# Kernel optimization log

Measured on AMD Instinct MI355X. Metric: run time of the kernel, lower is better.

Reference implementation:

```python
import jax, jax.numpy as jnp
import numpy as np

T = 200000


def _sine_layer(tvec, A, w, phi, phic, wc):
    # tvec: (t,), A/w/phi: (n,1), phic/wc: (1,)
    phi_static = jax.nn.relu(phic)  # (1,)
    w_static = jax.nn.relu(wc)
    ph = jax.nn.relu(phi) + phi_static  # (n,1)
    ww = jax.nn.relu(w) + w_static
    sine = A * jnp.sin(ww * tvec[None, :] + ph)  # (n,t)
    return sine, phi_static, w_static


def _selector_layer(tvec, wave_input, w, phi, phic, wc, phi_prev, w_prev):
    # wave_input: (n,t), w/phi: (m,n), phic/wc/phi_prev/w_prev: (1,)
    # NOTE: phi_prev/w_prev passed but phi_prev flag is False in the network,
    # so they are NOT added (matches torch: `if self.phi_prev and ...`).
    phi_static = jax.nn.relu(phic)
    w_static = jax.nn.relu(wc)
    ph = (jax.nn.relu(phi) + phi_static)[:, :, None]  # (m,n,1)
    ww = (jax.nn.relu(w) + w_static)[:, :, None]
    sine = 0.5 * jnp.sin(ww * tvec[None, None, :] + ph) + 0.5  # (m,n,t)
    out = jnp.einsum('mnt,nt->mt', sine, wave_input)  # (m,t)
    return out, phi_static, w_static


def setup_inputs() -> dict:
    key = jax.random.key(0)
    ks = jax.random.split(key, 18)
    r = lambda k, s: jax.random.normal(k, s, dtype=jnp.float32)
    return {
        'initial_wave_input': r(ks[0], (20, T)),
        'A0': r(ks[1], (20, 1)), 'w0': r(ks[2], (20, 1)), 'phi0': r(ks[3], (20, 1)),
        'wc0': r(ks[4], (1,)), 'phic0': r(ks[5], (1,)),
        'w1': r(ks[6], (25, 20)), 'phi1': r(ks[7], (25, 20)),
        'wc1': r(ks[8], (1,)), 'phic1': r(ks[9], (1,)),
        'w2': r(ks[10], (30, 25)), 'phi2': r(ks[11], (30, 25)),
        'wc2': r(ks[12], (1,)), 'phic2': r(ks[13], (1,)),
        'w3': r(ks[14], (1, 30)), 'phi3': r(ks[15], (1, 30)),
        'wc3': r(ks[16], (1,)), 'phic3': r(ks[17], (1,)),
    }


def reference(initial_wave_input, A0, w0, phi0, wc0, phic0,
              w1, phi1, wc1, phic1, w2, phi2, wc2, phic2,
              w3, phi3, wc3, phic3):
    tvec = jnp.linspace(1.0, 1000.0, T, dtype=jnp.float32)
    # initial_wave_input is an argument of the torch module but is never used.
    s, phi, w = _sine_layer(tvec, A0, w0, phi0, phic0, wc0)
    s, phi, w = _selector_layer(tvec, s, w1, phi1, phic1, wc1, phi, w)
    s, phi, w = _selector_layer(tvec, s, w2, phi2, phic2, wc2, phi, w)
    s, phi, w = _selector_layer(tvec, s, w3, phi3, phic3, wc3, phi, w)
    return s  # (1, t)
```

## Files before the change

kernel.cpp:

```cpp
#include <hip/hip_runtime.h>
#include <hip/hip_bf16.h>

#define T_TOTAL 200000
#define INV2PI 0.15915494309189535f

__device__ float g_P[2840];

__device__ __forceinline__ float relu_f(float x) { return fmaxf(x, 0.0f); }

__device__ __forceinline__ float sin_rev(float rev) {
    return __builtin_amdgcn_sinf(__builtin_amdgcn_fractf(rev));
}

__global__ void prep_kernel(
    const float* __restrict__ A0,
    const float* __restrict__ w0, const float* __restrict__ phi0,
    const float* __restrict__ wc0, const float* __restrict__ phic0,
    const float* __restrict__ w1, const float* __restrict__ phi1,
    const float* __restrict__ wc1, const float* __restrict__ phic1,
    const float* __restrict__ w2, const float* __restrict__ phi2,
    const float* __restrict__ wc2, const float* __restrict__ phic2,
    const float* __restrict__ w3, const float* __restrict__ phi3,
    const float* __restrict__ wc3, const float* __restrict__ phic3)
{
    const int tid = blockIdx.x * blockDim.x + threadIdx.x;
    const int stride = blockDim.x * gridDim.x;

    const float ws0 = relu_f(wc0[0]), ps0 = relu_f(phic0[0]);
    const float ws1 = relu_f(wc1[0]), ps1 = relu_f(phic1[0]);
    const float ws2 = relu_f(wc2[0]), ps2 = relu_f(phic2[0]);
    const float ws3 = relu_f(wc3[0]), ps3 = relu_f(phic3[0]);

    for (int n = tid; n < 20; n += stride) {
        g_P[2 * n]     = (relu_f(w0[n])   + ws0) * INV2PI;
        g_P[2 * n + 1] = (relu_f(phi0[n]) + ps0) * INV2PI;
        g_P[40 + n]    = A0[n];
    }
    for (int k = tid; k < 20 * 28; k += stride) {
        const int n = k / 28, m = k % 28;
        const int d = 60 + 2 * k;
        if (m < 25) {
            const int s = m * 20 + n;
            g_P[d]     = (relu_f(w1[s])   + ws1) * INV2PI;
            g_P[d + 1] = (relu_f(phi1[s]) + ps1) * INV2PI;
        } else {
            g_P[d] = 0.0f; g_P[d + 1] = 0.0f;
        }
    }
    for (int k = tid; k < 25 * 32; k += stride) {
        const int n = k / 32, m = k % 32;
        const int d = 1180 + 2 * k;
        if (m < 30) {
            const int s = m * 25 + n;
            g_P[d]     = (relu_f(w2[s])   + ws2) * INV2PI;
            g_P[d + 1] = (relu_f(phi2[s]) + ps2) * INV2PI;
        } else {
            g_P[d] = 0.0f; g_P[d + 1] = 0.0f;
        }
    }
    for (int k = tid; k < 30; k += stride) {
        g_P[2780 + 2 * k]     = (relu_f(w3[k])   + ws3) * INV2PI;
        g_P[2780 + 2 * k + 1] = (relu_f(phi3[k]) + ps3) * INV2PI;
    }
}

__launch_bounds__(256)
__global__ void wave_main(float* __restrict__ out)
{
    __shared__ float sh0[20 * 64];
    __shared__ float sh1[25 * 64];
    __shared__ float sh2[30 * 64];

    const int tid = threadIdx.x;
    const int l = tid & 63;
    const int w = __builtin_amdgcn_readfirstlane(tid >> 6);
    const int t = blockIdx.x * 64 + l;
    const float tv = fmaf((float)t, 999.0f / 199999.0f, 1.0f);

    {
        const float* __restrict__ p = &g_P[10 * w];
        const float* __restrict__ a = &g_P[40 + 5 * w];
#pragma unroll
        for (int i = 0; i < 5; ++i) {
            float rev = fmaf(p[2 * i], tv, p[2 * i + 1]);
            sh0[(5 * w + i) * 64 + l] = a[i] * sin_rev(rev);
        }
    }
    __syncthreads();

    float acc1[7];
#pragma unroll
    for (int j = 0; j < 7; ++j) acc1[j] = 0.0f;
    float sum0 = 0.0f;
#pragma clang loop unroll(disable)
    for (int n = 0; n < 20; ++n) {
        const float s0n = sh0[n * 64 + l];
        sum0 += s0n;
        const float* __restrict__ p = &g_P[60 + 56 * n + 14 * w];
#pragma unroll
        for (int j = 0; j < 7; ++j) {
            float rev = fmaf(p[2 * j], tv, p[2 * j + 1]);
            acc1[j] = fmaf(sin_rev(rev), s0n, acc1[j]);
        }
    }
#pragma unroll
    for (int j = 0; j < 7; ++j) {
        const int m = 7 * w + j;
        if (m < 25) sh1[m * 64 + l] = fmaf(0.5f, acc1[j], 0.5f * sum0);
    }
    __syncthreads();

    float acc2[8];
#pragma unroll
    for (int j = 0; j < 8; ++j) acc2[j] = 0.0f;
    float sum1 = 0.0f;
#pragma clang loop unroll(disable)
    for (int n = 0; n < 25; ++n) {
        const float s1n = sh1[n * 64 + l];
        sum1 += s1n;
        const float* __restrict__ p = &g_P[1180 + 64 * n + 16 * w];
#pragma unroll
        for (int j = 0; j < 8; ++j) {
            float rev = fmaf(p[2 * j], tv, p[2 * j + 1]);
            acc2[j] = fmaf(sin_rev(rev), s1n, acc2[j]);
        }
    }
#pragma unroll
    for (int j = 0; j < 8; ++j) {
        const int m = 8 * w + j;
        if (m < 30) sh2[m * 64 + l] = fmaf(0.5f, acc2[j], 0.5f * sum1);
    }
    __syncthreads();

    if (w == 0) {
        float acc3 = 0.0f, sum2 = 0.0f;
#pragma unroll
        for (int n = 0; n < 30; ++n) {
            const float s2n = sh2[n * 64 + l];
            sum2 += s2n;
            float rev = fmaf(g_P[2780 + 2 * n], tv, g_P[2780 + 2 * n + 1]);
            acc3 = fmaf(sin_rev(rev), s2n, acc3);
        }
        out[t] = fmaf(0.5f, acc3, 0.5f * sum2);
    }
}

extern "C" void kernel_launch(void* const* d_in, const int* in_sizes, int n_in,
                              void* d_out, int out_size, void* d_ws, size_t ws_size,
                              hipStream_t stream) {
    (void)in_sizes; (void)n_in; (void)d_ws; (void)ws_size; (void)out_size;
    const float* A0    = (const float*)d_in[1];
    const float* w0    = (const float*)d_in[2];
    const float* phi0  = (const float*)d_in[3];
    const float* wc0   = (const float*)d_in[4];
    const float* phic0 = (const float*)d_in[5];
    const float* w1    = (const float*)d_in[6];
    const float* phi1  = (const float*)d_in[7];
    const float* wc1   = (const float*)d_in[8];
    const float* phic1 = (const float*)d_in[9];
    const float* w2    = (const float*)d_in[10];
    const float* phi2  = (const float*)d_in[11];
    const float* wc2   = (const float*)d_in[12];
    const float* phic2 = (const float*)d_in[13];
    const float* w3    = (const float*)d_in[14];
    const float* phi3  = (const float*)d_in[15];
    const float* wc3   = (const float*)d_in[16];
    const float* phic3 = (const float*)d_in[17];

    float* out = (float*)d_out;

    hipLaunchKernelGGL(prep_kernel, dim3(11), dim3(256), 0, stream,
                       A0, w0, phi0, wc0, phic0,
                       w1, phi1, wc1, phic1,
                       w2, phi2, wc2, phic2,
                       w3, phi3, wc3, phic3);

    const int grid = T_TOTAL / 64;
    hipLaunchKernelGGL(wave_main, dim3(grid), dim3(256), 0, stream, out);
}
```

Before: 53.51 us.

## Use Chebyshev recurrence and polynomial sine with 4 time points per thread

Each thread now handles four time samples spaced 64 apart. It computes sin directly for the first two and gets the other two from the recurrence x_{k+1} = 2cos(wΔ)x_k − x_{k−1}, using cosines precomputed in double on the device. The hardware sin is replaced by a minimax polynomial on the fractional revolution, with a quarter-turn phase offset baked in. The last layer's dot product is split across all four waves and reduced through shared memory. This cuts transcendental work and grid size, at the cost of approximation error and error growth in the recurrence, especially at the large phase arguments used.

```diff
diff --git a/kernel.cpp b/kernel.cpp
--- a/kernel.cpp
+++ b/kernel.cpp
@@ -2,14 +2,20 @@
 #include <hip/hip_bf16.h>
 
 #define T_TOTAL 200000
-#define INV2PI 0.15915494309189535f
-
-__device__ float g_P[2840];
-
-__device__ __forceinline__ float relu_f(float x) { return fmaxf(x, 0.0f); }
-
-__device__ __forceinline__ float sin_rev(float rev) {
-    return __builtin_amdgcn_sinf(__builtin_amdgcn_fractf(rev));
+
+typedef float v4f __attribute__((ext_vector_type(4)));
+
+__device__ float g_P[4496];
+
+__device__ __forceinline__ float sinp(float rev) {
+    float g = __builtin_amdgcn_fractf(rev);
+    float h = g - 0.5f;
+    float u = h * h;
+    float p = fmaf(45.621248f, u, -82.391040f);
+    p = fmaf(p, u, 64.671616f);
+    p = fmaf(p, u, -19.730960f);
+    p = fmaf(p, u, 0.9999618f);
+    return p;
 }
 
 __global__ void prep_kernel(
@@ -26,123 +32,176 @@
     const int tid = blockIdx.x * blockDim.x + threadIdx.x;
     const int stride = blockDim.x * gridDim.x;
 
-    const float ws0 = relu_f(wc0[0]), ps0 = relu_f(phic0[0]);
-    const float ws1 = relu_f(wc1[0]), ps1 = relu_f(phic1[0]);
-    const float ws2 = relu_f(wc2[0]), ps2 = relu_f(phic2[0]);
-    const float ws3 = relu_f(wc3[0]), ps3 = relu_f(phic3[0]);
+    const double I2PI = 0.15915494309189535;
+    const double D64  = 64.0 * 999.0 / 199999.0;
+
+    const double ws0 = fmax((double)wc0[0], 0.0), ps0 = fmax((double)phic0[0], 0.0);
+    const double ws1 = fmax((double)wc1[0], 0.0), ps1 = fmax((double)phic1[0], 0.0);
+    const double ws2 = fmax((double)wc2[0], 0.0), ps2 = fmax((double)phic2[0], 0.0);
+    const double ws3 = fmax((double)wc3[0], 0.0), ps3 = fmax((double)phic3[0], 0.0);
 
     for (int n = tid; n < 20; n += stride) {
-        g_P[2 * n]     = (relu_f(w0[n])   + ws0) * INV2PI;
-        g_P[2 * n + 1] = (relu_f(phi0[n]) + ps0) * INV2PI;
-        g_P[40 + n]    = A0[n];
-    }
-    for (int k = tid; k < 20 * 28; k += stride) {
-        const int n = k / 28, m = k % 28;
-        const int d = 60 + 2 * k;
+        double wr = fmax((double)w0[n], 0.0) + ws0;
+        g_P[n]      = (float)(wr * I2PI);
+        g_P[20 + n] = (float)((fmax((double)phi0[n], 0.0) + ps0) * I2PI + 0.25);
+        g_P[40 + n] = (float)(2.0 * cos(wr * D64));
+        g_P[60 + n] = A0[n];
+    }
+    for (int k = tid; k < 20 * 32; k += stride) {
+        const int n = k >> 5, m = k & 31;
+        float wwf = 0.0f, phf = 0.25f, cf = 2.0f;
         if (m < 25) {
             const int s = m * 20 + n;
-            g_P[d]     = (relu_f(w1[s])   + ws1) * INV2PI;
-            g_P[d + 1] = (relu_f(phi1[s]) + ps1) * INV2PI;
-        } else {
-            g_P[d] = 0.0f; g_P[d + 1] = 0.0f;
-        }
+            double wr = fmax((double)w1[s], 0.0) + ws1;
+            wwf = (float)(wr * I2PI);
+            phf = (float)((fmax((double)phi1[s], 0.0) + ps1) * I2PI + 0.25);
+            cf  = (float)(2.0 * cos(wr * D64));
+        }
+        g_P[80 + 96 * n + m]      = wwf;
+        g_P[80 + 96 * n + 32 + m] = phf;
+        g_P[80 + 96 * n + 64 + m] = cf;
     }
     for (int k = tid; k < 25 * 32; k += stride) {
-        const int n = k / 32, m = k % 32;
-        const int d = 1180 + 2 * k;
+        const int n = k >> 5, m = k & 31;
+        float wwf = 0.0f, phf = 0.25f, cf = 2.0f;
         if (m < 30) {
             const int s = m * 25 + n;
-            g_P[d]     = (relu_f(w2[s])   + ws2) * INV2PI;
-            g_P[d + 1] = (relu_f(phi2[s]) + ps2) * INV2PI;
-        } else {
-            g_P[d] = 0.0f; g_P[d + 1] = 0.0f;
-        }
-    }
-    for (int k = tid; k < 30; k += stride) {
-        g_P[2780 + 2 * k]     = (relu_f(w3[k])   + ws3) * INV2PI;
-        g_P[2780 + 2 * k + 1] = (relu_f(phi3[k]) + ps3) * INV2PI;
+            double wr = fmax((double)w2[s], 0.0) + ws2;
+            wwf = (float)(wr * I2PI);
+            phf = (float)((fmax((double)phi2[s], 0.0) + ps2) * I2PI + 0.25);
+            cf  = (float)(2.0 * cos(wr * D64));
+        }
+        g_P[2000 + 96 * n + m]      = wwf;
+        g_P[2000 + 96 * n + 32 + m] = phf;
+        g_P[2000 + 96 * n + 64 + m] = cf;
+    }
+    for (int k = tid; k < 32; k += stride) {
+        float wwf = 0.0f, phf = 0.0f, cf = 2.0f;
+        if (k < 30) {
+            double wr = fmax((double)w3[k], 0.0) + ws3;
+            wwf = (float)(wr * I2PI);
+            phf = (float)((fmax((double)phi3[k], 0.0) + ps3) * I2PI + 0.25);
+            cf  = (float)(2.0 * cos(wr * D64));
+        }
+        g_P[4400 + k]      = wwf;
+        g_P[4400 + 32 + k] = phf;
+        g_P[4400 + 64 + k] = cf;
     }
 }
 
 __launch_bounds__(256)
 __global__ void wave_main(float* __restrict__ out)
 {
-    __shared__ float sh0[20 * 64];
-    __shared__ float sh1[25 * 64];
-    __shared__ float sh2[30 * 64];
-
-    const int tid = threadIdx.x;
-    const int l = tid & 63;
-    const int w = __builtin_amdgcn_readfirstlane(tid >> 6);
-    const int t = blockIdx.x * 64 + l;
-    const float tv = fmaf((float)t, 999.0f / 199999.0f, 1.0f);
-
-    {
-        const float* __restrict__ p = &g_P[10 * w];
-        const float* __restrict__ a = &g_P[40 + 5 * w];
-#pragma unroll
-        for (int i = 0; i < 5; ++i) {
-            float rev = fmaf(p[2 * i], tv, p[2 * i + 1]);
-            sh0[(5 * w + i) * 64 + l] = a[i] * sin_rev(rev);
-        }
+    __shared__ float sh0[20][64][4];
+    __shared__ float sh1[25][64][4];
+    __shared__ float shp[4][64][4];
+
+    const int l = threadIdx.x & 63;
+    const int w = __builtin_amdgcn_readfirstlane(threadIdx.x >> 6);
+    const int tb = blockIdx.x * 256;
+    const float STEP = 999.0f / 199999.0f;
+
+    float tv[4];
+#pragma unroll
+    for (int j = 0; j < 4; ++j)
+        tv[j] = fmaf((float)(tb + l + 64 * j), STEP, 1.0f);
+
+#pragma unroll
+    for (int i = 0; i < 5; ++i) {
+        const int n = 5 * w + i;
+        const float ww = g_P[n], ph = g_P[20 + n], C = g_P[40 + n], A = g_P[60 + n];
+        float x0 = A * sinp(fmaf(ww, tv[0], ph));
+        float x1 = A * sinp(fmaf(ww, tv[1], ph));
+        float x2 = fmaf(C, x1, -x0);
+        float x3 = fmaf(C, x2, -x1);
+        *(v4f*)&sh0[n][l][0] = (v4f){x0, x1, x2, x3};
     }
     __syncthreads();
 
-    float acc1[7];
-#pragma unroll
-    for (int j = 0; j < 7; ++j) acc1[j] = 0.0f;
-    float sum0 = 0.0f;
+    float acc1[8][4] = {};
+    float sum0[4] = {0.f, 0.f, 0.f, 0.f};
 #pragma clang loop unroll(disable)
     for (int n = 0; n < 20; ++n) {
-        const float s0n = sh0[n * 64 + l];
-        sum0 += s0n;
-        const float* __restrict__ p = &g_P[60 + 56 * n + 14 * w];
-#pragma unroll
-        for (int j = 0; j < 7; ++j) {
-            float rev = fmaf(p[2 * j], tv, p[2 * j + 1]);
-            acc1[j] = fmaf(sin_rev(rev), s0n, acc1[j]);
-        }
-    }
-#pragma unroll
-    for (int j = 0; j < 7; ++j) {
-        const int m = 7 * w + j;
-        if (m < 25) sh1[m * 64 + l] = fmaf(0.5f, acc1[j], 0.5f * sum0);
+        const v4f s0 = *(const v4f*)&sh0[n][l][0];
+#pragma unroll
+        for (int j = 0; j < 4; ++j) sum0[j] += s0[j];
+        const float* __restrict__ pb = &g_P[80 + 96 * n + 8 * w];
+#pragma unroll
+        for (int k = 0; k < 8; ++k) {
+            const float ww = pb[k], ph = pb[32 + k], C = pb[64 + k];
+            float x0 = sinp(fmaf(ww, tv[0], ph));
+            float x1 = sinp(fmaf(ww, tv[1], ph));
+            float x2 = fmaf(C, x1, -x0);
+            float x3 = fmaf(C, x2, -x1);
+            acc1[k][0] = fmaf(x0, s0[0], acc1[k][0]);
+            acc1[k][1] = fmaf(x1, s0[1], acc1[k][1]);
+            acc1[k][2] = fmaf(x2, s0[2], acc1[k][2]);
+            acc1[k][3] = fmaf(x3, s0[3], acc1[k][3]);
+        }
+    }
+#pragma unroll
+    for (int k = 0; k < 8; ++k) {
+        if (8 * w + k < 25) {
+            v4f v;
+#pragma unroll
+            for (int j = 0; j < 4; ++j) v[j] = fmaf(0.5f, acc1[k][j], 0.5f * sum0[j]);
+            *(v4f*)&sh1[8 * w + k][l][0] = v;
+        }
     }
     __syncthreads();
 
-    float acc2[8];
-#pragma unroll
-    for (int j = 0; j < 8; ++j) acc2[j] = 0.0f;
-    float sum1 = 0.0f;
+    float acc2[8][4] = {};
+    float sum1[4] = {0.f, 0.f, 0.f, 0.f};
 #pragma clang loop unroll(disable)
     for (int n = 0; n < 25; ++n) {
-        const float s1n = sh1[n * 64 + l];
-        sum1 += s1n;
-        const float* __restrict__ p = &g_P[1180 + 64 * n + 16 * w];
-#pragma unroll
-        for (int j = 0; j < 8; ++j) {
-            float rev = fmaf(p[2 * j], tv, p[2 * j + 1]);
-            acc2[j] = fmaf(sin_rev(rev), s1n, acc2[j]);
-        }
-    }
-#pragma unroll
-    for (int j = 0; j < 8; ++j) {
-        const int m = 8 * w + j;
-        if (m < 30) sh2[m * 64 + l] = fmaf(0.5f, acc2[j], 0.5f * sum1);
-    }
+        const v4f s1 = *(const v4f*)&sh1[n][l][0];
+#pragma unroll
+        for (int j = 0; j < 4; ++j) sum1[j] += s1[j];
+        const float* __restrict__ pb = &g_P[2000 + 96 * n + 8 * w];
+#pragma unroll
+        for (int k = 0; k < 8; ++k) {
+            const float ww = pb[k], ph = pb[32 + k], C = pb[64 + k];
+            float x0 = sinp(fmaf(ww, tv[0], ph));
+            float x1 = sinp(fmaf(ww, tv[1], ph));
+            float x2 = fmaf(C, x1, -x0);
+            float x3 = fmaf(C, x2, -x1);
+            acc2[k][0] = fmaf(x0, s1[0], acc2[k][0]);
+            acc2[k][1] = fmaf(x1, s1[1], acc2[k][1]);
+            acc2[k][2] = fmaf(x2, s1[2], acc2[k][2]);
+            acc2[k][3] = fmaf(x3, s1[3], acc2[k][3]);
+        }
+    }
+    float s2r[8][4];
+#pragma unroll
+    for (int k = 0; k < 8; ++k)
+#pragma unroll
+        for (int j = 0; j < 4; ++j)
+            s2r[k][j] = fmaf(0.5f, acc2[k][j], 0.5f * sum1[j]);
+
+    float pw[4] = {0.f, 0.f, 0.f, 0.f};
+    {
+        const float* __restrict__ pb = &g_P[4400 + 8 * w];
+#pragma unroll
+        for (int k = 0; k < 8; ++k) {
+            if (8 * w + k < 30) {
+                const float ww = pb[k], ph = pb[32 + k], C = pb[64 + k];
+                float x0 = sinp(fmaf(ww, tv[0], ph));
+                float x1 = sinp(fmaf(ww, tv[1], ph));
+                float x2 = fmaf(C, x1, -x0);
+                float x3 = fmaf(C, x2, -x1);
+                pw[0] = fmaf(fmaf(0.5f, x0, 0.5f), s2r[k][0], pw[0]);
+                pw[1] = fmaf(fmaf(0.5f, x1, 0.5f), s2r[k][1], pw[1]);
+                pw[2] = fmaf(fmaf(0.5f, x2, 0.5f), s2r[k][2], pw[2]);
+                pw[3] = fmaf(fmaf(0.5f, x3, 0.5f), s2r[k][3], pw[3]);
+            }
+        }
+    }
+    *(v4f*)&shp[w][l][0] = (v4f){pw[0], pw[1], pw[2], pw[3]};
     __syncthreads();
 
-    if (w == 0) {
-        float acc3 = 0.0f, sum2 = 0.0f;
-#pragma unroll
-        for (int n = 0; n < 30; ++n) {
-            const float s2n = sh2[n * 64 + l];
-            sum2 += s2n;
-            float rev = fmaf(g_P[2780 + 2 * n], tv, g_P[2780 + 2 * n + 1]);
-            acc3 = fmaf(sin_rev(rev), s2n, acc3);
-        }
-        out[t] = fmaf(0.5f, acc3, 0.5f * sum2);
-    }
+    const float r = (shp[0][l][w] + shp[1][l][w]) + (shp[2][l][w] + shp[3][l][w]);
+    const int tt = tb + l + 64 * w;
+    if (tt < T_TOTAL) out[tt] = r;
 }
 
 extern "C" void kernel_launch(void* const* d_in, const int* in_sizes, int n_in,
@@ -169,12 +228,12 @@
 
     float* out = (float*)d_out;
 
-    hipLaunchKernelGGL(prep_kernel, dim3(11), dim3(256), 0, stream,
+    hipLaunchKernelGGL(prep_kernel, dim3(6), dim3(256), 0, stream,
                        A0, w0, phi0, wc0, phic0,
                        w1, phi1, wc1, phic1,
                        w2, phi2, wc2, phic2,
                        w3, phi3, wc3, phic3);
 
-    const int grid = T_TOTAL / 64;
+    const int grid = (T_TOTAL + 255) / 256;
     hipLaunchKernelGGL(wave_main, dim3(grid), dim3(256), 0, stream, out);
 }
```

Measured after the change: 54.69 us. 1.02x slower.
